# Optimization experiments

Hardware: AMD Instinct MI355X
Metric: run time of the kernel (lower is better)

## Reference

```python
import jax, jax.numpy as jnp
import numpy as np

N_USERS = 200000
N_ITEMS = 100000
EMB_DIM = 64
N_LAYERS = 3
N_EDGES = 4000000
N_TOTAL = N_USERS + N_ITEMS


def setup_inputs() -> dict:
    key = jax.random.key(0)
    k1, k2, k3, k4 = jax.random.split(key, 4)
    # Xavier-uniform-ish init scale for embeddings
    lim = float(np.sqrt(6.0 / (N_USERS + EMB_DIM)))
    user_w = jax.random.uniform(k1, (N_USERS, EMB_DIM), jnp.float32, -lim, lim)
    lim_i = float(np.sqrt(6.0 / (N_ITEMS + EMB_DIM)))
    item_w = jax.random.uniform(k2, (N_ITEMS, EMB_DIM), jnp.float32, -lim_i, lim_i)
    src = jax.random.randint(k3, (N_EDGES,), 0, N_TOTAL, dtype=jnp.int32)
    dst = jax.random.randint(k4, (N_EDGES,), 0, N_TOTAL, dtype=jnp.int32)
    return {"user_w": user_w, "item_w": item_w, "src": src, "dst": dst}


def reference(user_w, item_w, src, dst):
    # x: [N_TOTAL, D] joint node embedding table
    x = jnp.concatenate([user_w, item_w], axis=0)
    # Row-degree of the COO adjacency (duplicates sum, same as coalesce)
    deg = jax.ops.segment_sum(jnp.ones_like(src, dtype=x.dtype), src,
                              num_segments=N_TOTAL)
    deg_inv_sqrt = jax.lax.rsqrt(deg + 1e-8)
    # Symmetric normalization weight per edge: d_i^-1/2 * d_j^-1/2
    w = (deg_inv_sqrt[src] * deg_inv_sqrt[dst])[:, None]  # [E, 1]

    h = x
    acc = x
    for _ in range(N_LAYERS):
        # SpMM: out[i] = sum_{(i,j) in E} w_ij * h[j]
        h = jax.ops.segment_sum(w * h[dst], src, num_segments=N_TOTAL)
        acc = acc + h
    out = acc / (N_LAYERS + 1)
    return out[:N_USERS], out[N_USERS:]
```

## Files before the change

### kernel.cpp

```cpp
#include <hip/hip_runtime.h>

#define N_USERS  200000
#define N_ITEMS  100000
#define N_TOTAL  300000
#define EMB_DIM  64
#define N_EDGES  4000000
#define N_LAYERS 3

#define SCAN_CHUNK 1024

#define B2_BITS 9
#define B2_ROWS (1 << B2_BITS)
#define NB2 ((N_TOTAL + B2_ROWS - 1) >> B2_BITS)
#define CHUNK_E 8192
#define NBLK ((N_EDGES + CHUNK_E - 1) / CHUNK_E)
#define NFLAT (NB2 * NBLK)
#define NSB_FLAT ((NFLAT + SCAN_CHUNK - 1) / SCAN_CHUNK)

#define DST_BITS 19
#define DST_MASK ((1 << DST_BITS) - 1)

#define P2_CAP 10240

#define GR 4

typedef float f32x2 __attribute__((ext_vector_type(2)));

__device__ __forceinline__ unsigned bfpack(float a, float b) {
    unsigned ua = __float_as_uint(a); ua = (ua + 0x7fffu + ((ua >> 16) & 1u)) >> 16;
    unsigned ub = __float_as_uint(b); ub = (ub + 0x7fffu + ((ub >> 16) & 1u)) >> 16;
    return ua | (ub << 16);
}
__device__ __forceinline__ float bflo(unsigned u) { return __uint_as_float(u << 16); }
__device__ __forceinline__ float bfhi(unsigned u) { return __uint_as_float(u & 0xffff0000u); }
__device__ __forceinline__ f32x2 bf2(unsigned u) {
    f32x2 t; t.x = bflo(u); t.y = bfhi(u); return t;
}

__global__ void scanA_g(const int* __restrict__ in, int* __restrict__ out,
                        int* __restrict__ bsums, int n) {
    __shared__ int lds[256];
    int t = threadIdx.x, b = blockIdx.x;
    int base = b * SCAN_CHUNK + t * 4;
    int v[4];
#pragma unroll
    for (int k = 0; k < 4; ++k)
        v[k] = (base + k < n) ? in[base + k] : 0;
    int s = v[0] + v[1] + v[2] + v[3];
    lds[t] = s;
    __syncthreads();
    for (int off = 1; off < 256; off <<= 1) {
        int x = (t >= off) ? lds[t - off] : 0;
        __syncthreads();
        lds[t] += x;
        __syncthreads();
    }
    int inc = lds[t];
    int exc = inc - s;
    if (t == 255) bsums[b] = inc;
    int run = exc;
#pragma unroll
    for (int k = 0; k < 4; ++k) {
        if (base + k < n) out[base + k] = run;
        run += v[k];
    }
}

__global__ void scanB_g(int* __restrict__ bsums, int nb, int* __restrict__ total_out) {
    __shared__ int lds[512];
    int t = threadIdx.x;
    int v = (t < nb) ? bsums[t] : 0;
    lds[t] = v;
    __syncthreads();
    for (int o = 1; o < 512; o <<= 1) {
        int x = (t >= o) ? lds[t - o] : 0;
        __syncthreads();
        lds[t] += x;
        __syncthreads();
    }
    if (t < nb) bsums[t] = lds[t] - v;
    if (total_out && t == nb - 1) *total_out = lds[t];
}

__global__ __launch_bounds__(512) void partA_kernel(const int* __restrict__ src,
                                                    int* __restrict__ bcnt) {
    __shared__ int lcnt[NB2];
    int blk = blockIdx.x, t = threadIdx.x;
    for (int i = t; i < NB2; i += 512) lcnt[i] = 0;
    __syncthreads();
    int base = blk * CHUNK_E;
    int end = base + CHUNK_E; if (end > N_EDGES) end = N_EDGES;
    for (int e = base + 4 * t; e < end; e += 4 * 512) {
        int4 s4 = *(const int4*)(src + e);
        atomicAdd(&lcnt[s4.x >> B2_BITS], 1);
        atomicAdd(&lcnt[s4.y >> B2_BITS], 1);
        atomicAdd(&lcnt[s4.z >> B2_BITS], 1);
        atomicAdd(&lcnt[s4.w >> B2_BITS], 1);
    }
    __syncthreads();
    for (int i = t; i < NB2; i += 512)
        bcnt[(size_t)i * NBLK + blk] = lcnt[i];
}

__global__ __launch_bounds__(512) void partC_kernel(const int* __restrict__ src,
                                                    const int* __restrict__ dst,
                                                    const int* __restrict__ boffs,
                                                    const int* __restrict__ bs2,
                                                    int* __restrict__ edgebuf) {
    __shared__ int lcur[NB2];
    int blk = blockIdx.x, t = threadIdx.x;
    for (int i = t; i < NB2; i += 512) {
        size_t f = (size_t)i * NBLK + blk;
        lcur[i] = boffs[f] + bs2[f >> 10];
    }
    __syncthreads();
    int base = blk * CHUNK_E;
    int end = base + CHUNK_E; if (end > N_EDGES) end = N_EDGES;
    for (int e = base + 2 * t; e < end; e += 2 * 512) {
        int2 s2 = *(const int2*)(src + e);
        int2 d2 = *(const int2*)(dst + e);
        int pos0 = atomicAdd(&lcur[s2.x >> B2_BITS], 1);
        edgebuf[pos0] = ((s2.x & (B2_ROWS - 1)) << DST_BITS) | d2.x;
        int pos1 = atomicAdd(&lcur[s2.y >> B2_BITS], 1);
        edgebuf[pos1] = ((s2.y & (B2_ROWS - 1)) << DST_BITS) | d2.y;
    }
}

__global__ __launch_bounds__(512) void part2_kernel(const int* __restrict__ boffs,
                                                    const int* __restrict__ bs2,
                                                    const int* __restrict__ edgebuf,
                                                    int* __restrict__ col,
                                                    int* __restrict__ offs,
                                                    float* __restrict__ dinv) {
    __shared__ int lhist[B2_ROWS];
    __shared__ int lsums[512];
    __shared__ int lbuf[P2_CAP];
    int b = blockIdx.x;
    int base = b << B2_BITS;
    int nrows = N_TOTAL - base; if (nrows > B2_ROWS) nrows = B2_ROWS;
    int t = threadIdx.x;
    size_t f0 = (size_t)b * NBLK;
    int bstart = boffs[f0] + bs2[f0 >> 10];
    int eend;
    if (b + 1 < NB2) {
        size_t f1 = (size_t)(b + 1) * NBLK;
        eend = boffs[f1] + bs2[f1 >> 10];
    } else eend = N_EDGES;
    int cnt = eend - bstart;
    bool fits = (cnt <= P2_CAP);

    if (t < B2_ROWS) lhist[t] = 0;
    __syncthreads();
    if (fits) {
        for (int j = t; j < cnt; j += 512) {
            int e = edgebuf[bstart + j];
            lbuf[j] = e;
            atomicAdd(&lhist[e >> DST_BITS], 1);
        }
    } else {
        for (int j = bstart + t; j < eend; j += 512)
            atomicAdd(&lhist[edgebuf[j] >> DST_BITS], 1);
    }
    __syncthreads();
    int v = lhist[t];
    lsums[t] = v;
    __syncthreads();
    for (int o = 1; o < 512; o <<= 1) {
        int x = (t >= o) ? lsums[t - o] : 0;
        __syncthreads();
        lsums[t] += x;
        __syncthreads();
    }
    int o0 = bstart + lsums[t] - v;
    if (t < nrows) {
        offs[base + t] = o0;
        dinv[base + t] = rsqrtf((float)v + 1e-8f);
    }
    if (b == NB2 - 1 && t == 0) offs[N_TOTAL] = N_EDGES;
    lhist[t] = o0;
    __syncthreads();
    if (fits) {
        for (int j = t; j < cnt; j += 512) {
            int e = lbuf[j];
            int pos = atomicAdd(&lhist[e >> DST_BITS], 1);
            col[pos] = e & DST_MASK;
        }
    } else {
        for (int j = bstart + t; j < eend; j += 512) {
            int e = edgebuf[j];
            int pos = atomicAdd(&lhist[e >> DST_BITS], 1);
            col[pos] = e & DST_MASK;
        }
    }
}

__global__ void convert_kernel(const float4* __restrict__ uw4,
                               const float4* __restrict__ iw4,
                               const float* __restrict__ dinv,
                               uint2* __restrict__ g0) {
    int i = blockIdx.x * blockDim.x + threadIdx.x;
    const int n = (N_TOTAL + 1) * 16;
    if (i < n) {
        int row = i >> 4;
        if (row >= N_TOTAL) {
            g0[i] = make_uint2(0u, 0u);
        } else {
            float4 x = (row < N_USERS) ? uw4[i] : iw4[i - N_USERS * 16];
            float di = dinv[row];
            g0[i] = make_uint2(bfpack(di * x.x, di * x.y),
                               bfpack(di * x.z, di * x.w));
        }
    }
}

template <int MODE>
__global__ __launch_bounds__(256) void gather_kernel(
        const int* __restrict__ offs,
        const int* __restrict__ col,
        const float* __restrict__ dinv,
        const unsigned* __restrict__ gprev,
        unsigned* __restrict__ gnext,
        float4* __restrict__ out4,
        const float4* __restrict__ uw4,
        const float4* __restrict__ iw4) {
    int wid  = blockIdx.x * 4 + (threadIdx.x >> 6);
    int base_row = wid * GR;
    int lane = threadIdx.x & 63;
    int q    = lane >> 4;
    int r    = lane & 15;
    int li = lane < GR ? lane : GR;
    int off_l = offs[base_row + li];
    float dv  = dinv[base_row + (lane < GR ? lane : GR - 1)];

    int s0 = __builtin_amdgcn_readlane(off_l, 0);
    int e0 = __builtin_amdgcn_readlane(off_l, 1);
    int myc_cur = (lane < e0 - s0) ? col[s0 + lane] : N_TOTAL;

#pragma unroll
    for (int i = 0; i < GR; ++i) {
        int start = __builtin_amdgcn_readlane(off_l, i);
        int end   = __builtin_amdgcn_readlane(off_l, i + 1);
        int myc_next = N_TOTAL;
        if (i + 1 < GR) {
            int sn = __builtin_amdgcn_readlane(off_l, i + 1);
            int en = __builtin_amdgcn_readlane(off_l, i + 2);
            myc_next = (lane < en - sn) ? col[sn + lane] : N_TOTAL;
        }
        f32x2 acc01 = {0.f, 0.f};
        f32x2 acc23 = {0.f, 0.f};
        int n = end - start; if (n > 64) n = 64;
        for (int k0 = 0; k0 < n; k0 += 16) {
            int c0 = __shfl(myc_cur, k0 + q);
            int c1 = __shfl(myc_cur, k0 + 4 + q);
            int c2 = __shfl(myc_cur, k0 + 8 + q);
            int c3 = __shfl(myc_cur, k0 + 12 + q);
            uint2 u0 = *(const uint2*)(gprev + ((size_t)(unsigned)c0 << 5) + 2 * r);
            uint2 u1 = *(const uint2*)(gprev + ((size_t)(unsigned)c1 << 5) + 2 * r);
            uint2 u2 = *(const uint2*)(gprev + ((size_t)(unsigned)c2 << 5) + 2 * r);
            uint2 u3 = *(const uint2*)(gprev + ((size_t)(unsigned)c3 << 5) + 2 * r);
            acc01 += bf2(u0.x); acc23 += bf2(u0.y);
            acc01 += bf2(u1.x); acc23 += bf2(u1.y);
            acc01 += bf2(u2.x); acc23 += bf2(u2.y);
            acc01 += bf2(u3.x); acc23 += bf2(u3.y);
        }
        for (int cb = start + 64; cb < end; cb += 64) {
            int rem = end - cb;
            int nn = rem > 64 ? 64 : rem;
            int myc = (lane < rem) ? col[cb + lane] : N_TOTAL;
            for (int k0 = 0; k0 < nn; k0 += 16) {
                int c0 = __shfl(myc, k0 + q);
                int c1 = __shfl(myc, k0 + 4 + q);
                int c2 = __shfl(myc, k0 + 8 + q);
                int c3 = __shfl(myc, k0 + 12 + q);
                uint2 u0 = *(const uint2*)(gprev + ((size_t)(unsigned)c0 << 5) + 2 * r);
                uint2 u1 = *(const uint2*)(gprev + ((size_t)(unsigned)c1 << 5) + 2 * r);
                uint2 u2 = *(const uint2*)(gprev + ((size_t)(unsigned)c2 << 5) + 2 * r);
                uint2 u3 = *(const uint2*)(gprev + ((size_t)(unsigned)c3 << 5) + 2 * r);
                acc01 += bf2(u0.x); acc23 += bf2(u0.y);
                acc01 += bf2(u1.x); acc23 += bf2(u1.y);
                acc01 += bf2(u2.x); acc23 += bf2(u2.y);
                acc01 += bf2(u3.x); acc23 += bf2(u3.y);
            }
        }
        float a0 = acc01.x, a1 = acc01.y, a2 = acc23.x, a3 = acc23.y;
        a0 += __shfl_xor(a0, 16);
        a1 += __shfl_xor(a1, 16);
        a2 += __shfl_xor(a2, 16);
        a3 += __shfl_xor(a3, 16);
        a0 += __shfl_xor(a0, 32);
        a1 += __shfl_xor(a1, 32);
        a2 += __shfl_xor(a2, 32);
        a3 += __shfl_xor(a3, 32);
        float di = __shfl(dv, i);
        if (lane < 16) {
            int row = base_row + i;
            float h0 = di * a0, h1 = di * a1, h2 = di * a2, h3 = di * a3;
            int p = row * 16 + r;
            if (MODE == 0) {
                float4 x = (row < N_USERS) ? uw4[p] : iw4[p - N_USERS * 16];
                ((uint2*)gnext)[p] = make_uint2(bfpack(di * h0, di * h1),
                                                bfpack(di * h2, di * h3));
                out4[p] = make_float4(x.x + h0, x.y + h1, x.z + h2, x.w + h3);
            } else if (MODE == 1) {
                float4 o = out4[p];
                ((uint2*)gnext)[p] = make_uint2(bfpack(di * h0, di * h1),
                                                bfpack(di * h2, di * h3));
                out4[p] = make_float4(o.x + h0, o.y + h1, o.z + h2, o.w + h3);
            } else {
                float4 o = out4[p];
                out4[p] = make_float4((o.x + h0) * 0.25f, (o.y + h1) * 0.25f,
                                      (o.z + h2) * 0.25f, (o.w + h3) * 0.25f);
            }
        }
        myc_cur = myc_next;
    }
    if (MODE != 2) {
        if (blockIdx.x == 0 && threadIdx.x < 32)
            gnext[N_TOTAL * 32 + threadIdx.x] = 0u;
    }
}

extern "C" void kernel_launch(void* const* d_in, const int* in_sizes, int n_in,
                              void* d_out, int out_size, void* d_ws, size_t ws_size,
                              hipStream_t stream) {
    const float* user_w = (const float*)d_in[0];
    const float* item_w = (const float*)d_in[1];
    const int*   src    = (const int*)d_in[2];
    const int*   dst    = (const int*)d_in[3];
    float* out = (float*)d_out;
    (void)in_sizes; (void)n_in; (void)out_size; (void)ws_size;

    char* ws = (char*)d_ws;
    size_t off = 0;
    auto alloc = [&](size_t bytes) {
        char* p = ws + off;
        off = (off + bytes + 255) & ~(size_t)255;
        return p;
    };
    int*      offs   = (int*)     alloc((size_t)(N_TOTAL + 1) * 4);
    int*      bcnt   = (int*)     alloc((size_t)NFLAT * 4);
    int*      boffs  = (int*)     alloc((size_t)NFLAT * 4);
    int*      bs2    = (int*)     alloc((size_t)NSB_FLAT * 4);
    int*      col    = (int*)     alloc((size_t)N_EDGES * 4);
    int*      edgebuf= (int*)     alloc((size_t)N_EDGES * 4);
    float*    dinv   = (float*)   alloc((size_t)N_TOTAL * 4);
    unsigned* g0     = (unsigned*)alloc((size_t)(N_TOTAL + 1) * 32 * 4);
    unsigned* g_a    = (unsigned*)alloc((size_t)(N_TOTAL + 1) * 32 * 4);
    unsigned* g_b    = (unsigned*)alloc((size_t)(N_TOTAL + 1) * 32 * 4);

    const int B = 256;
    const int gatherGrid = N_TOTAL / (4 * GR);

    partA_kernel<<<NBLK, 512, 0, stream>>>(src, bcnt);
    scanA_g<<<NSB_FLAT, B, 0, stream>>>(bcnt, boffs, bs2, NFLAT);
    scanB_g<<<1, 512, 0, stream>>>(bs2, NSB_FLAT, nullptr);
    partC_kernel<<<NBLK, 512, 0, stream>>>(src, dst, boffs, bs2, edgebuf);
    part2_kernel<<<NB2, 512, 0, stream>>>(boffs, bs2, edgebuf, col, offs, dinv);

    convert_kernel<<<((N_TOTAL + 1) * 16 + B - 1) / B, B, 0, stream>>>(
        (const float4*)user_w, (const float4*)item_w, dinv, (uint2*)g0);

    const float4* uw4 = (const float4*)user_w;
    const float4* iw4 = (const float4*)item_w;
    float4* out4 = (float4*)out;
    gather_kernel<0><<<gatherGrid, B, 0, stream>>>(offs, col, dinv, g0,  g_a, out4, uw4, iw4);
    gather_kernel<1><<<gatherGrid, B, 0, stream>>>(offs, col, dinv, g_a, g_b, out4, uw4, iw4);
    gather_kernel<2><<<gatherGrid, B, 0, stream>>>(offs, col, dinv, g_b, nullptr, out4, uw4, iw4);
}
```

Baseline: 535.7 us.

## Process four rows per wave concurrently in gather and halve partition chunk size

Result: slower. 549.5 us (+2.6%).

```diff
diff --git a/kernel.cpp b/kernel.cpp
--- a/kernel.cpp
+++ b/kernel.cpp
@@ -12,7 +12,7 @@
 #define B2_BITS 9
 #define B2_ROWS (1 << B2_BITS)
 #define NB2 ((N_TOTAL + B2_ROWS - 1) >> B2_BITS)
-#define CHUNK_E 8192
+#define CHUNK_E 4096
 #define NBLK ((N_EDGES + CHUNK_E - 1) / CHUNK_E)
 #define NFLAT (NB2 * NBLK)
 #define NSB_FLAT ((NFLAT + SCAN_CHUNK - 1) / SCAN_CHUNK)
@@ -22,7 +22,7 @@
 
 #define P2_CAP 10240
 
-#define GR 4
+#define GROWS 16
 
 typedef float f32x2 __attribute__((ext_vector_type(2)));
 
@@ -66,11 +66,13 @@
     }
 }
 
-__global__ void scanB_g(int* __restrict__ bsums, int nb, int* __restrict__ total_out) {
+__global__ void scanB_g(int* __restrict__ bsums, int nb) {
     __shared__ int lds[512];
     int t = threadIdx.x;
-    int v = (t < nb) ? bsums[t] : 0;
-    lds[t] = v;
+    int v0 = (2 * t < nb) ? bsums[2 * t] : 0;
+    int v1 = (2 * t + 1 < nb) ? bsums[2 * t + 1] : 0;
+    int s = v0 + v1;
+    lds[t] = s;
     __syncthreads();
     for (int o = 1; o < 512; o <<= 1) {
         int x = (t >= o) ? lds[t - o] : 0;
@@ -78,8 +80,9 @@
         lds[t] += x;
         __syncthreads();
     }
-    if (t < nb) bsums[t] = lds[t] - v;
-    if (total_out && t == nb - 1) *total_out = lds[t];
+    int exc = lds[t] - s;
+    if (2 * t < nb) bsums[2 * t] = exc;
+    if (2 * t + 1 < nb) bsums[2 * t + 1] = exc + v0;
 }
 
 __global__ __launch_bounds__(512) void partA_kernel(const int* __restrict__ src,
@@ -224,77 +227,61 @@
         const float4* __restrict__ uw4,
         const float4* __restrict__ iw4) {
     int wid  = blockIdx.x * 4 + (threadIdx.x >> 6);
-    int base_row = wid * GR;
+    int base = wid * GROWS;
     int lane = threadIdx.x & 63;
     int q    = lane >> 4;
     int r    = lane & 15;
-    int li = lane < GR ? lane : GR;
-    int off_l = offs[base_row + li];
-    float dv  = dinv[base_row + (lane < GR ? lane : GR - 1)];
-
-    int s0 = __builtin_amdgcn_readlane(off_l, 0);
-    int e0 = __builtin_amdgcn_readlane(off_l, 1);
-    int myc_cur = (lane < e0 - s0) ? col[s0 + lane] : N_TOTAL;
-
+    if (base < N_TOTAL) {
+        int   off_l = offs[base + (lane < GROWS + 1 ? lane : GROWS)];
+        float dv_l  = dinv[base + r];
+        int s_l = __shfl(off_l, q);
+        int e_l = __shfl(off_l, q + 1);
+        int myc_cur = (r < e_l - s_l) ? col[s_l + r] : N_TOTAL;
 #pragma unroll
-    for (int i = 0; i < GR; ++i) {
-        int start = __builtin_amdgcn_readlane(off_l, i);
-        int end   = __builtin_amdgcn_readlane(off_l, i + 1);
-        int myc_next = N_TOTAL;
-        if (i + 1 < GR) {
-            int sn = __builtin_amdgcn_readlane(off_l, i + 1);
-            int en = __builtin_amdgcn_readlane(off_l, i + 2);
-            myc_next = (lane < en - sn) ? col[sn + lane] : N_TOTAL;
-        }
-        f32x2 acc01 = {0.f, 0.f};
-        f32x2 acc23 = {0.f, 0.f};
-        int n = end - start; if (n > 64) n = 64;
-        for (int k0 = 0; k0 < n; k0 += 16) {
-            int c0 = __shfl(myc_cur, k0 + q);
-            int c1 = __shfl(myc_cur, k0 + 4 + q);
-            int c2 = __shfl(myc_cur, k0 + 8 + q);
-            int c3 = __shfl(myc_cur, k0 + 12 + q);
-            uint2 u0 = *(const uint2*)(gprev + ((size_t)(unsigned)c0 << 5) + 2 * r);
-            uint2 u1 = *(const uint2*)(gprev + ((size_t)(unsigned)c1 << 5) + 2 * r);
-            uint2 u2 = *(const uint2*)(gprev + ((size_t)(unsigned)c2 << 5) + 2 * r);
-            uint2 u3 = *(const uint2*)(gprev + ((size_t)(unsigned)c3 << 5) + 2 * r);
-            acc01 += bf2(u0.x); acc23 += bf2(u0.y);
-            acc01 += bf2(u1.x); acc23 += bf2(u1.y);
-            acc01 += bf2(u2.x); acc23 += bf2(u2.y);
-            acc01 += bf2(u3.x); acc23 += bf2(u3.y);
-        }
-        for (int cb = start + 64; cb < end; cb += 64) {
-            int rem = end - cb;
-            int nn = rem > 64 ? 64 : rem;
-            int myc = (lane < rem) ? col[cb + lane] : N_TOTAL;
-            for (int k0 = 0; k0 < nn; k0 += 16) {
-                int c0 = __shfl(myc, k0 + q);
-                int c1 = __shfl(myc, k0 + 4 + q);
-                int c2 = __shfl(myc, k0 + 8 + q);
-                int c3 = __shfl(myc, k0 + 12 + q);
-                uint2 u0 = *(const uint2*)(gprev + ((size_t)(unsigned)c0 << 5) + 2 * r);
-                uint2 u1 = *(const uint2*)(gprev + ((size_t)(unsigned)c1 << 5) + 2 * r);
-                uint2 u2 = *(const uint2*)(gprev + ((size_t)(unsigned)c2 << 5) + 2 * r);
-                uint2 u3 = *(const uint2*)(gprev + ((size_t)(unsigned)c3 << 5) + 2 * r);
-                acc01 += bf2(u0.x); acc23 += bf2(u0.y);
-                acc01 += bf2(u1.x); acc23 += bf2(u1.y);
-                acc01 += bf2(u2.x); acc23 += bf2(u2.y);
-                acc01 += bf2(u3.x); acc23 += bf2(u3.y);
+        for (int j = 0; j < GROWS / 4; ++j) {
+            int o0 = __builtin_amdgcn_readlane(off_l, 4 * j);
+            int o1 = __builtin_amdgcn_readlane(off_l, 4 * j + 1);
+            int o2 = __builtin_amdgcn_readlane(off_l, 4 * j + 2);
+            int o3 = __builtin_amdgcn_readlane(off_l, 4 * j + 3);
+            int o4 = __builtin_amdgcn_readlane(off_l, 4 * j + 4);
+            int kmax = max(max(o1 - o0, o2 - o1), max(o3 - o2, o4 - o3));
+            int s_lane = __shfl(off_l, 4 * j + q);
+            int n_lane = __shfl(off_l, 4 * j + q + 1) - s_lane;
+            int myc_next = N_TOTAL;
+            if (j + 1 < GROWS / 4) {
+                int sn = __shfl(off_l, 4 * (j + 1) + q);
+                int en = __shfl(off_l, 4 * (j + 1) + q + 1);
+                myc_next = (r < en - sn) ? col[sn + r] : N_TOTAL;
             }
-        }
-        float a0 = acc01.x, a1 = acc01.y, a2 = acc23.x, a3 = acc23.y;
-        a0 += __shfl_xor(a0, 16);
-        a1 += __shfl_xor(a1, 16);
-        a2 += __shfl_xor(a2, 16);
-        a3 += __shfl_xor(a3, 16);
-        a0 += __shfl_xor(a0, 32);
-        a1 += __shfl_xor(a1, 32);
-        a2 += __shfl_xor(a2, 32);
-        a3 += __shfl_xor(a3, 32);
-        float di = __shfl(dv, i);
-        if (lane < 16) {
-            int row = base_row + i;
-            float h0 = di * a0, h1 = di * a1, h2 = di * a2, h3 = di * a3;
+            f32x2 acc01 = {0.f, 0.f};
+            f32x2 acc23 = {0.f, 0.f};
+            int myc = myc_cur;
+            for (int w0 = 0; w0 < kmax; w0 += 16) {
+                int kw = kmax - w0; if (kw > 16) kw = 16;
+                for (int k = 0; k < kw; k += 4) {
+                    int bl = (q << 4) + k;
+                    int c0 = __shfl(myc, bl);
+                    int c1 = __shfl(myc, bl + 1);
+                    int c2 = __shfl(myc, bl + 2);
+                    int c3 = __shfl(myc, bl + 3);
+                    uint2 u0 = *(const uint2*)(gprev + ((size_t)(unsigned)c0 << 5) + 2 * r);
+                    uint2 u1 = *(const uint2*)(gprev + ((size_t)(unsigned)c1 << 5) + 2 * r);
+                    uint2 u2 = *(const uint2*)(gprev + ((size_t)(unsigned)c2 << 5) + 2 * r);
+                    uint2 u3 = *(const uint2*)(gprev + ((size_t)(unsigned)c3 << 5) + 2 * r);
+                    acc01 += bf2(u0.x); acc23 += bf2(u0.y);
+                    acc01 += bf2(u1.x); acc23 += bf2(u1.y);
+                    acc01 += bf2(u2.x); acc23 += bf2(u2.y);
+                    acc01 += bf2(u3.x); acc23 += bf2(u3.y);
+                }
+                if (w0 + 16 < kmax) {
+                    int o = w0 + 16;
+                    myc = (o + r < n_lane) ? col[s_lane + o + r] : N_TOTAL;
+                }
+            }
+            float di = __shfl(dv_l, 4 * j + q);
+            int row = base + 4 * j + q;
+            float h0 = di * acc01.x, h1 = di * acc01.y;
+            float h2 = di * acc23.x, h3 = di * acc23.y;
             int p = row * 16 + r;
             if (MODE == 0) {
                 float4 x = (row < N_USERS) ? uw4[p] : iw4[p - N_USERS * 16];
@@ -311,8 +298,8 @@
                 out4[p] = make_float4((o.x + h0) * 0.25f, (o.y + h1) * 0.25f,
                                       (o.z + h2) * 0.25f, (o.w + h3) * 0.25f);
             }
-        }
-        myc_cur = myc_next;
+            myc_cur = myc_next;
+        }
     }
     if (MODE != 2) {
         if (blockIdx.x == 0 && threadIdx.x < 32)
@@ -349,11 +336,12 @@
     unsigned* g_b    = (unsigned*)alloc((size_t)(N_TOTAL + 1) * 32 * 4);
 
     const int B = 256;
-    const int gatherGrid = N_TOTAL / (4 * GR);
+    const int nWaves = (N_TOTAL + GROWS - 1) / GROWS;
+    const int gatherGrid = (nWaves + 3) / 4;
 
     partA_kernel<<<NBLK, 512, 0, stream>>>(src, bcnt);
     scanA_g<<<NSB_FLAT, B, 0, stream>>>(bcnt, boffs, bs2, NFLAT);
-    scanB_g<<<1, 512, 0, stream>>>(bs2, NSB_FLAT, nullptr);
+    scanB_g<<<1, 512, 0, stream>>>(bs2, NSB_FLAT);
     partC_kernel<<<NBLK, 512, 0, stream>>>(src, dst, boffs, bs2, edgebuf);
     part2_kernel<<<NB2, 512, 0, stream>>>(boffs, bs2, edgebuf, col, offs, dinv);
 
```

## Single-pass bucket partition with fixed-capacity buckets and fused bf16 conversion

Applied to the files above, without the earlier changes.

New measurement: 538.0 us. No clear change (+0.4%).

```diff
diff --git a/kernel.cpp b/kernel.cpp
--- a/kernel.cpp
+++ b/kernel.cpp
@@ -7,20 +7,16 @@
 #define N_EDGES  4000000
 #define N_LAYERS 3
 
-#define SCAN_CHUNK 1024
-
 #define B2_BITS 9
 #define B2_ROWS (1 << B2_BITS)
 #define NB2 ((N_TOTAL + B2_ROWS - 1) >> B2_BITS)
 #define CHUNK_E 8192
 #define NBLK ((N_EDGES + CHUNK_E - 1) / CHUNK_E)
-#define NFLAT (NB2 * NBLK)
-#define NSB_FLAT ((NFLAT + SCAN_CHUNK - 1) / SCAN_CHUNK)
+#define BCAP_BITS 13
+#define BCAP (1 << BCAP_BITS)
 
 #define DST_BITS 19
 #define DST_MASK ((1 << DST_BITS) - 1)
-
-#define P2_CAP 10240
 
 #define GR 4
 
@@ -37,40 +33,56 @@
     f32x2 t; t.x = bflo(u); t.y = bfhi(u); return t;
 }
 
-__global__ void scanA_g(const int* __restrict__ in, int* __restrict__ out,
-                        int* __restrict__ bsums, int n) {
-    __shared__ int lds[256];
-    int t = threadIdx.x, b = blockIdx.x;
-    int base = b * SCAN_CHUNK + t * 4;
-    int v[4];
-#pragma unroll
-    for (int k = 0; k < 4; ++k)
-        v[k] = (base + k < n) ? in[base + k] : 0;
-    int s = v[0] + v[1] + v[2] + v[3];
-    lds[t] = s;
-    __syncthreads();
-    for (int off = 1; off < 256; off <<= 1) {
-        int x = (t >= off) ? lds[t - off] : 0;
-        __syncthreads();
-        lds[t] += x;
-        __syncthreads();
-    }
-    int inc = lds[t];
-    int exc = inc - s;
-    if (t == 255) bsums[b] = inc;
-    int run = exc;
-#pragma unroll
-    for (int k = 0; k < 4; ++k) {
-        if (base + k < n) out[base + k] = run;
-        run += v[k];
-    }
-}
-
-__global__ void scanB_g(int* __restrict__ bsums, int nb, int* __restrict__ total_out) {
+__global__ __launch_bounds__(512) void part1_kernel(const int* __restrict__ src,
+                                                    const int* __restrict__ dst,
+                                                    int* __restrict__ gcur,
+                                                    int* __restrict__ edgebuf) {
+    __shared__ int lcnt[NB2];
+    __shared__ int lcur[NB2];
+    __shared__ int ssrc[CHUNK_E];
+    int blk = blockIdx.x, t = threadIdx.x;
+    for (int i = t; i < NB2; i += 512) lcnt[i] = 0;
+    __syncthreads();
+    int base = blk * CHUNK_E;
+    int end = base + CHUNK_E; if (end > N_EDGES) end = N_EDGES;
+    for (int e = base + 4 * t; e < end; e += 4 * 512) {
+        int4 s4 = *(const int4*)(src + e);
+        *(int4*)(ssrc + (e - base)) = s4;
+        atomicAdd(&lcnt[s4.x >> B2_BITS], 1);
+        atomicAdd(&lcnt[s4.y >> B2_BITS], 1);
+        atomicAdd(&lcnt[s4.z >> B2_BITS], 1);
+        atomicAdd(&lcnt[s4.w >> B2_BITS], 1);
+    }
+    __syncthreads();
+    for (int i = t; i < NB2; i += 512) {
+        int c = lcnt[i];
+        int b0 = c ? atomicAdd(&gcur[i], c) : 0;
+        lcur[i] = (i << BCAP_BITS) + b0;
+    }
+    __syncthreads();
+    for (int e = base + 4 * t; e < end; e += 4 * 512) {
+        int4 d4 = *(const int4*)(dst + e);
+        int j = e - base;
+        int s0 = ssrc[j], s1 = ssrc[j + 1], s2 = ssrc[j + 2], s3 = ssrc[j + 3];
+        int p0 = atomicAdd(&lcur[s0 >> B2_BITS], 1);
+        edgebuf[p0] = ((s0 & (B2_ROWS - 1)) << DST_BITS) | d4.x;
+        int p1 = atomicAdd(&lcur[s1 >> B2_BITS], 1);
+        edgebuf[p1] = ((s1 & (B2_ROWS - 1)) << DST_BITS) | d4.y;
+        int p2 = atomicAdd(&lcur[s2 >> B2_BITS], 1);
+        edgebuf[p2] = ((s2 & (B2_ROWS - 1)) << DST_BITS) | d4.z;
+        int p3 = atomicAdd(&lcur[s3 >> B2_BITS], 1);
+        edgebuf[p3] = ((s3 & (B2_ROWS - 1)) << DST_BITS) | d4.w;
+    }
+}
+
+__global__ void scanT_kernel(const int* __restrict__ gcur, int* __restrict__ bbase,
+                             unsigned* __restrict__ g0) {
     __shared__ int lds[512];
     int t = threadIdx.x;
-    int v = (t < nb) ? bsums[t] : 0;
-    lds[t] = v;
+    int v0 = (2 * t < NB2) ? gcur[2 * t] : 0;
+    int v1 = (2 * t + 1 < NB2) ? gcur[2 * t + 1] : 0;
+    int s = v0 + v1;
+    lds[t] = s;
     __syncthreads();
     for (int o = 1; o < 512; o <<= 1) {
         int x = (t >= o) ? lds[t - o] : 0;
@@ -78,88 +90,39 @@
         lds[t] += x;
         __syncthreads();
     }
-    if (t < nb) bsums[t] = lds[t] - v;
-    if (total_out && t == nb - 1) *total_out = lds[t];
-}
-
-__global__ __launch_bounds__(512) void partA_kernel(const int* __restrict__ src,
-                                                    int* __restrict__ bcnt) {
-    __shared__ int lcnt[NB2];
-    int blk = blockIdx.x, t = threadIdx.x;
-    for (int i = t; i < NB2; i += 512) lcnt[i] = 0;
-    __syncthreads();
-    int base = blk * CHUNK_E;
-    int end = base + CHUNK_E; if (end > N_EDGES) end = N_EDGES;
-    for (int e = base + 4 * t; e < end; e += 4 * 512) {
-        int4 s4 = *(const int4*)(src + e);
-        atomicAdd(&lcnt[s4.x >> B2_BITS], 1);
-        atomicAdd(&lcnt[s4.y >> B2_BITS], 1);
-        atomicAdd(&lcnt[s4.z >> B2_BITS], 1);
-        atomicAdd(&lcnt[s4.w >> B2_BITS], 1);
-    }
-    __syncthreads();
-    for (int i = t; i < NB2; i += 512)
-        bcnt[(size_t)i * NBLK + blk] = lcnt[i];
-}
-
-__global__ __launch_bounds__(512) void partC_kernel(const int* __restrict__ src,
-                                                    const int* __restrict__ dst,
-                                                    const int* __restrict__ boffs,
-                                                    const int* __restrict__ bs2,
-                                                    int* __restrict__ edgebuf) {
-    __shared__ int lcur[NB2];
-    int blk = blockIdx.x, t = threadIdx.x;
-    for (int i = t; i < NB2; i += 512) {
-        size_t f = (size_t)i * NBLK + blk;
-        lcur[i] = boffs[f] + bs2[f >> 10];
-    }
-    __syncthreads();
-    int base = blk * CHUNK_E;
-    int end = base + CHUNK_E; if (end > N_EDGES) end = N_EDGES;
-    for (int e = base + 2 * t; e < end; e += 2 * 512) {
-        int2 s2 = *(const int2*)(src + e);
-        int2 d2 = *(const int2*)(dst + e);
-        int pos0 = atomicAdd(&lcur[s2.x >> B2_BITS], 1);
-        edgebuf[pos0] = ((s2.x & (B2_ROWS - 1)) << DST_BITS) | d2.x;
-        int pos1 = atomicAdd(&lcur[s2.y >> B2_BITS], 1);
-        edgebuf[pos1] = ((s2.y & (B2_ROWS - 1)) << DST_BITS) | d2.y;
-    }
-}
-
-__global__ __launch_bounds__(512) void part2_kernel(const int* __restrict__ boffs,
-                                                    const int* __restrict__ bs2,
+    int exc = lds[t] - s;
+    if (2 * t < NB2) bbase[2 * t] = exc;
+    if (2 * t + 1 < NB2) bbase[2 * t + 1] = exc + v0;
+    if (t == 511) bbase[NB2] = lds[511];
+    if (t < 32) g0[(size_t)N_TOTAL * 32 + t] = 0u;
+}
+
+__global__ __launch_bounds__(512) void part2_kernel(const int* __restrict__ gcur,
+                                                    const int* __restrict__ bbase,
                                                     const int* __restrict__ edgebuf,
                                                     int* __restrict__ col,
                                                     int* __restrict__ offs,
-                                                    float* __restrict__ dinv) {
+                                                    float* __restrict__ dinv,
+                                                    const float4* __restrict__ uw4,
+                                                    const float4* __restrict__ iw4,
+                                                    uint2* __restrict__ g0) {
     __shared__ int lhist[B2_ROWS];
     __shared__ int lsums[512];
-    __shared__ int lbuf[P2_CAP];
+    __shared__ int lbuf[BCAP];
     int b = blockIdx.x;
     int base = b << B2_BITS;
     int nrows = N_TOTAL - base; if (nrows > B2_ROWS) nrows = B2_ROWS;
     int t = threadIdx.x;
-    size_t f0 = (size_t)b * NBLK;
-    int bstart = boffs[f0] + bs2[f0 >> 10];
-    int eend;
-    if (b + 1 < NB2) {
-        size_t f1 = (size_t)(b + 1) * NBLK;
-        eend = boffs[f1] + bs2[f1 >> 10];
-    } else eend = N_EDGES;
-    int cnt = eend - bstart;
-    bool fits = (cnt <= P2_CAP);
-
-    if (t < B2_ROWS) lhist[t] = 0;
-    __syncthreads();
-    if (fits) {
-        for (int j = t; j < cnt; j += 512) {
-            int e = edgebuf[bstart + j];
-            lbuf[j] = e;
-            atomicAdd(&lhist[e >> DST_BITS], 1);
-        }
-    } else {
-        for (int j = bstart + t; j < eend; j += 512)
-            atomicAdd(&lhist[edgebuf[j] >> DST_BITS], 1);
+    int cnt    = gcur[b];
+    int bstart = bbase[b];
+    int ebase  = b << BCAP_BITS;
+
+    lhist[t] = 0;
+    __syncthreads();
+    for (int j = t; j < cnt; j += 512) {
+        int e = edgebuf[ebase + j];
+        lbuf[j] = e;
+        atomicAdd(&lhist[e >> DST_BITS], 1);
     }
     __syncthreads();
     int v = lhist[t];
@@ -172,44 +135,30 @@
         __syncthreads();
     }
     int o0 = bstart + lsums[t] - v;
+    float dv = rsqrtf((float)v + 1e-8f);
     if (t < nrows) {
         offs[base + t] = o0;
-        dinv[base + t] = rsqrtf((float)v + 1e-8f);
+        dinv[base + t] = dv;
     }
     if (b == NB2 - 1 && t == 0) offs[N_TOTAL] = N_EDGES;
+    __syncthreads();
     lhist[t] = o0;
-    __syncthreads();
-    if (fits) {
-        for (int j = t; j < cnt; j += 512) {
-            int e = lbuf[j];
-            int pos = atomicAdd(&lhist[e >> DST_BITS], 1);
-            col[pos] = e & DST_MASK;
-        }
-    } else {
-        for (int j = bstart + t; j < eend; j += 512) {
-            int e = edgebuf[j];
-            int pos = atomicAdd(&lhist[e >> DST_BITS], 1);
-            col[pos] = e & DST_MASK;
-        }
-    }
-}
-
-__global__ void convert_kernel(const float4* __restrict__ uw4,
-                               const float4* __restrict__ iw4,
-                               const float* __restrict__ dinv,
-                               uint2* __restrict__ g0) {
-    int i = blockIdx.x * blockDim.x + threadIdx.x;
-    const int n = (N_TOTAL + 1) * 16;
-    if (i < n) {
-        int row = i >> 4;
-        if (row >= N_TOTAL) {
-            g0[i] = make_uint2(0u, 0u);
-        } else {
-            float4 x = (row < N_USERS) ? uw4[i] : iw4[i - N_USERS * 16];
-            float di = dinv[row];
-            g0[i] = make_uint2(bfpack(di * x.x, di * x.y),
-                               bfpack(di * x.z, di * x.w));
-        }
+    lsums[t] = __float_as_int(dv);
+    __syncthreads();
+    for (int j = t; j < cnt; j += 512) {
+        int e = lbuf[j];
+        int pos = atomicAdd(&lhist[e >> DST_BITS], 1);
+        col[pos] = e & DST_MASK;
+    }
+    int np = nrows << 4;
+    for (int p = t; p < np; p += 512) {
+        int rl = p >> 4, rr = p & 15;
+        int row = base + rl;
+        float di = __int_as_float(lsums[rl]);
+        float4 x = (row < N_USERS) ? uw4[row * 16 + rr]
+                                   : iw4[(row - N_USERS) * 16 + rr];
+        g0[row * 16 + rr] = make_uint2(bfpack(di * x.x, di * x.y),
+                                       bfpack(di * x.z, di * x.w));
     }
 }
 
@@ -316,7 +265,7 @@
     }
     if (MODE != 2) {
         if (blockIdx.x == 0 && threadIdx.x < 32)
-            gnext[N_TOTAL * 32 + threadIdx.x] = 0u;
+            gnext[(size_t)N_TOTAL * 32 + threadIdx.x] = 0u;
     }
 }
 
@@ -337,13 +286,12 @@
         off = (off + bytes + 255) & ~(size_t)255;
         return p;
     };
+    int*      gcur   = (int*)     alloc((size_t)NB2 * 4);
+    int*      bbase  = (int*)     alloc((size_t)(NB2 + 1) * 4);
     int*      offs   = (int*)     alloc((size_t)(N_TOTAL + 1) * 4);
-    int*      bcnt   = (int*)     alloc((size_t)NFLAT * 4);
-    int*      boffs  = (int*)     alloc((size_t)NFLAT * 4);
-    int*      bs2    = (int*)     alloc((size_t)NSB_FLAT * 4);
+    float*    dinv   = (float*)   alloc((size_t)N_TOTAL * 4);
     int*      col    = (int*)     alloc((size_t)N_EDGES * 4);
-    int*      edgebuf= (int*)     alloc((size_t)N_EDGES * 4);
-    float*    dinv   = (float*)   alloc((size_t)N_TOTAL * 4);
+    int*      edgebuf= (int*)     alloc((size_t)NB2 * BCAP * 4);
     unsigned* g0     = (unsigned*)alloc((size_t)(N_TOTAL + 1) * 32 * 4);
     unsigned* g_a    = (unsigned*)alloc((size_t)(N_TOTAL + 1) * 32 * 4);
     unsigned* g_b    = (unsigned*)alloc((size_t)(N_TOTAL + 1) * 32 * 4);
@@ -351,18 +299,16 @@
     const int B = 256;
     const int gatherGrid = N_TOTAL / (4 * GR);
 
-    partA_kernel<<<NBLK, 512, 0, stream>>>(src, bcnt);
-    scanA_g<<<NSB_FLAT, B, 0, stream>>>(bcnt, boffs, bs2, NFLAT);
-    scanB_g<<<1, 512, 0, stream>>>(bs2, NSB_FLAT, nullptr);
-    partC_kernel<<<NBLK, 512, 0, stream>>>(src, dst, boffs, bs2, edgebuf);
-    part2_kernel<<<NB2, 512, 0, stream>>>(boffs, bs2, edgebuf, col, offs, dinv);
-
-    convert_kernel<<<((N_TOTAL + 1) * 16 + B - 1) / B, B, 0, stream>>>(
-        (const float4*)user_w, (const float4*)item_w, dinv, (uint2*)g0);
-
     const float4* uw4 = (const float4*)user_w;
     const float4* iw4 = (const float4*)item_w;
     float4* out4 = (float4*)out;
+
+    hipMemsetAsync(gcur, 0, (size_t)NB2 * 4, stream);
+    part1_kernel<<<NBLK, 512, 0, stream>>>(src, dst, gcur, edgebuf);
+    scanT_kernel<<<1, 512, 0, stream>>>(gcur, bbase, g0);
+    part2_kernel<<<NB2, 512, 0, stream>>>(gcur, bbase, edgebuf, col, offs, dinv,
+                                          uw4, iw4, (uint2*)g0);
+
     gather_kernel<0><<<gatherGrid, B, 0, stream>>>(offs, col, dinv, g0,  g_a, out4, uw4, iw4);
     gather_kernel<1><<<gatherGrid, B, 0, stream>>>(offs, col, dinv, g_a, g_b, out4, uw4, iw4);
     gather_kernel<2><<<gatherGrid, B, 0, stream>>>(offs, col, dinv, g_b, nullptr, out4, uw4, iw4);
```
